# Kernel tuning notes

Hardware: AMD Instinct MI355X
Metric: run time of the kernel (lower is better)

The kernel has to match this reference:

```python
import jax, jax.numpy as jnp
import numpy as np
import math

H = 1024
E = 8
K = 2
CF = 1.5
THR = 0.5


def setup_inputs() -> dict:
    key = jax.random.key(0)
    ks = jax.random.split(key, 8)
    s = 0.02
    return {
        'hidden_states': jax.random.normal(ks[0], (2, 2048, H), jnp.float32),
        # importance predictor: Linear(H, H//2) -> ReLU -> Linear(H//2, 1) -> Sigmoid
        'wi1': jax.random.normal(ks[1], (H, H // 2), jnp.float32) * s,
        'bi1': jnp.zeros((H // 2,), jnp.float32),
        'wi2': jax.random.normal(ks[2], (H // 2, 1), jnp.float32) * s,
        'bi2': jnp.zeros((1,), jnp.float32),
        # router_important: Linear(H,H) -> ReLU -> Linear(H,E)
        'wr1': jax.random.normal(ks[3], (H, H), jnp.float32) * s,
        'br1': jnp.zeros((H,), jnp.float32),
        'wr2': jax.random.normal(ks[4], (H, E), jnp.float32) * s,
        'br2': jnp.zeros((E,), jnp.float32),
        # router_unimportant: Linear(H,H) -> ReLU -> Linear(H,E)
        'wu1': jax.random.normal(ks[5], (H, H), jnp.float32) * s,
        'bu1': jnp.zeros((H,), jnp.float32),
        'wu2': jax.random.normal(ks[6], (H, E), jnp.float32) * s,
        'bu2': jnp.zeros((E,), jnp.float32),
    }


def reference(hidden_states, wi1, bi1, wi2, bi2, wr1, br1, wr2, br2, wu1, bu1, wu2, bu2):
    x = hidden_states
    B, S, _ = x.shape
    N = B * S
    capacity = int(B * S * CF * K / E)  # static per-expert capacity

    # dual-gate routing
    importance = jax.nn.sigmoid(jnp.maximum(x @ wi1 + bi1, 0.0) @ wi2 + bi2)  # [B,S,1]
    imp_mask = (importance > THR).astype(x.dtype)                              # [B,S,1]
    logits_imp = jnp.maximum(x @ wr1 + br1, 0.0) @ wr2 + br2                   # [B,S,E]
    logits_unimp = jnp.maximum(x @ wu1 + bu1, 0.0) @ wu2 + bu2                 # [B,S,E]
    router_logits = imp_mask * logits_imp + (1.0 - imp_mask) * logits_unimp
    router_probs = jax.nn.softmax(router_logits, axis=-1)                      # [B,S,E]

    top_k_probs, top_k_indices = jax.lax.top_k(router_probs, K)
    top_k_probs = top_k_probs / top_k_probs.sum(-1, keepdims=True)

    # capacity-constrained dispatch: k-major assignment order (outer loop over k,
    # tokens in order), position within expert = running count, drop if >= capacity
    ef = top_k_indices.reshape(N, K).T.reshape(-1)   # [K*N] expert id, k-major
    pf = top_k_probs.reshape(N, K).T.reshape(-1)     # [K*N] gate prob
    tf = jnp.tile(jnp.arange(N), K)                  # [K*N] token id
    oh = jax.nn.one_hot(ef, E, dtype=jnp.int32)      # [K*N, E]
    pos = jnp.take_along_axis(jnp.cumsum(oh, axis=0), ef[:, None], 1)[:, 0] - 1
    keep = pos < capacity
    posc = jnp.clip(pos, 0, capacity - 1)

    zeros = jnp.zeros((N, E, capacity), x.dtype)
    dispatch = zeros.at[tf, ef, posc].add(keep.astype(x.dtype))
    combine = zeros.at[tf, ef, posc].add(jnp.where(keep, pf, 0.0))
    dispatch = dispatch.reshape(B, S, E, capacity)
    combine = combine.reshape(B, S, E, capacity)

    # aux losses
    rppe = router_probs.mean((0, 1))
    entropy_loss = jnp.sum(rppe * jnp.log(rppe * E + 1e-9))
    imp_sum = (router_probs * imp_mask).sum((0, 1)) + 1e-9
    ippe = imp_sum / imp_sum.sum()
    imp_entropy = -jnp.sum(ippe * jnp.log(ippe + 1e-9))
    aux_loss = entropy_loss - 0.1 * (imp_entropy / math.log(E))

    return dispatch, combine, router_probs, aux_loss, importance
```

## Files before the change

### kernel.cpp

```cpp
#include <hip/hip_runtime.h>
#include <math.h>

#define HDIM  1024
#define HHALF 512
#define NEXP  8
#define NTOK  4096
#define CAP   1536
#define NTOT  2560
#define TOTAL_DC (2u * NTOK * NEXP * CAP)

typedef _Float16 f16x8 __attribute__((ext_vector_type(8)));
typedef float    f32x4 __attribute__((ext_vector_type(4)));

#define GEMM_BLOCKS 640
#define FILL_BLOCKS 1408
#define S_LO 2048.0f
#define S_W  32.0f

__global__ __launch_bounds__(256) void prep(
    const float* __restrict__ x,
    const float* __restrict__ wi1, const float* __restrict__ wr1,
    const float* __restrict__ wu1,
    const float* __restrict__ bi1, const float* __restrict__ br1,
    const float* __restrict__ bu1,
    _Float16* __restrict__ Ah, _Float16* __restrict__ Al,
    _Float16* __restrict__ Bth, _Float16* __restrict__ Btl,
    float* __restrict__ bias_cat)
{
    __shared__ float tile[64][65];
    const int bid = blockIdx.x, tid = threadIdx.x;

    if (bid < 2048) {
        const int i8 = bid * 256 + tid;
        const float4* x4 = (const float4*)x;
        float4 v0 = x4[i8 * 2];
        float4 v1 = x4[i8 * 2 + 1];
        float f[8] = {v0.x, v0.y, v0.z, v0.w, v1.x, v1.y, v1.z, v1.w};
        f16x8 hi, lo;
#pragma unroll
        for (int j = 0; j < 8; j++) {
            _Float16 h = (_Float16)f[j];
            hi[j] = h;
            lo[j] = (_Float16)((f[j] - (float)h) * S_LO);
        }
        *(f16x8*)&Ah[(size_t)i8 * 8] = hi;
        *(f16x8*)&Al[(size_t)i8 * 8] = lo;
        return;
    }
    if (bid < 2688) {
        int local; const float* src; int C, nof;
        int b = bid - 2048;
        if (b < 128)      { src = wi1; C = 512;  nof = 0;    local = b; }
        else if (b < 384) { src = wr1; C = 1024; nof = 512;  local = b - 128; }
        else              { src = wu1; C = 1024; nof = 1536; local = b - 384; }
        const int nti = local >> 4, kti = local & 15;
#pragma unroll
        for (int p = 0; p < 16; p++) {
            int e = p * 256 + tid;
            int kr = e >> 6, nc = e & 63;
            tile[kr][nc] = src[(size_t)(kti * 64 + kr) * C + nti * 64 + nc];
        }
        __syncthreads();
#pragma unroll
        for (int p = 0; p < 16; p++) {
            int e = p * 256 + tid;
            int nl = e >> 6, kk = e & 63;
            float w32 = tile[kk][nl] * S_W;
            _Float16 h = (_Float16)w32;
            _Float16 l = (_Float16)((w32 - (float)h) * S_LO);
            const size_t o = (size_t)(nof + nti * 64 + nl) * 1024 + kti * 64 + kk;
            Bth[o] = h;
            Btl[o] = l;
        }
        return;
    }
    for (int i = tid; i < NTOT; i += 256) {
        float v = (i < 512) ? bi1[i] : (i < 1536) ? br1[i - 512] : bu1[i - 1536];
        bias_cat[i] = v;
    }
}

__global__ __launch_bounds__(256, 2) void gemm_fill(
    const _Float16* __restrict__ Ah, const _Float16* __restrict__ Al,
    const _Float16* __restrict__ Bth, const _Float16* __restrict__ Btl,
    const float* __restrict__ bias_cat, float* __restrict__ H,
    float* __restrict__ out)
{
    if (blockIdx.x >= GEMM_BLOCKS) {
        float4* o4 = (float4*)out;
        const unsigned total4 = TOTAL_DC / 4;
        unsigned i = (blockIdx.x - GEMM_BLOCKS) * 256u + threadIdx.x;
        const unsigned stride = FILL_BLOCKS * 256u;
        const float4 z = {0.f, 0.f, 0.f, 0.f};
        for (; i < total4; i += stride) o4[i] = z;
        return;
    }

    __shared__ _Float16 lds[4][128][32];

    const int tid = threadIdx.x;
    const int lane = tid & 63, wid = tid >> 6;
    const int bn = blockIdx.x % 20, bm = blockIdx.x / 20;
    const int rowBase = bm * 128, colBase = bn * 128;

    const _Float16* gb =
        (wid == 0) ? Ah  + (size_t)rowBase * 1024 :
        (wid == 1) ? Al  + (size_t)rowBase * 1024 :
        (wid == 2) ? Bth + (size_t)colBase * 1024 :
                     Btl + (size_t)colBase * 1024;
    const int lrow = lane >> 2;
    const int lkg  = lane & 3;

    f32x4 acc_hh[4][4], acc_x[4][4];
    const f32x4 z4 = {0.f, 0.f, 0.f, 0.f};
#pragma unroll
    for (int i = 0; i < 4; i++)
#pragma unroll
        for (int j = 0; j < 4; j++) { acc_hh[i][j] = z4; acc_x[i][j] = z4; }

    const int mw = (wid >> 1) * 64, nw = (wid & 1) * 64;
    const int fr = lane & 15, s = lane >> 4;

    for (int k0 = 0; k0 < 1024; k0 += 32) {
        __syncthreads();
#pragma unroll
        for (int i = 0; i < 8; i++) {
            const int r = i * 16 + lrow;
            __builtin_amdgcn_global_load_lds(
                (const void*)(gb + (size_t)r * 1024 + k0 + lkg * 8),
                (void*)&lds[wid][i * 16][0], 16, 0, 0);
        }
        __syncthreads();

        f16x8 fa_h[4], fa_l[4], fb_h[4], fb_l[4];
#pragma unroll
        for (int mf = 0; mf < 4; mf++) {
            fa_h[mf] = *(const f16x8*)&lds[0][mw + mf * 16 + fr][s * 8];
            fa_l[mf] = *(const f16x8*)&lds[1][mw + mf * 16 + fr][s * 8];
        }
#pragma unroll
        for (int nf = 0; nf < 4; nf++) {
            fb_h[nf] = *(const f16x8*)&lds[2][nw + nf * 16 + fr][s * 8];
            fb_l[nf] = *(const f16x8*)&lds[3][nw + nf * 16 + fr][s * 8];
        }
#pragma unroll
        for (int mf = 0; mf < 4; mf++)
#pragma unroll
            for (int nf = 0; nf < 4; nf++) {
                acc_hh[mf][nf] = __builtin_amdgcn_mfma_f32_16x16x32_f16(
                    fa_h[mf], fb_h[nf], acc_hh[mf][nf], 0, 0, 0);
                acc_x[mf][nf] = __builtin_amdgcn_mfma_f32_16x16x32_f16(
                    fa_h[mf], fb_l[nf], acc_x[mf][nf], 0, 0, 0);
                acc_x[mf][nf] = __builtin_amdgcn_mfma_f32_16x16x32_f16(
                    fa_l[mf], fb_h[nf], acc_x[mf][nf], 0, 0, 0);
            }
    }

#pragma unroll
    for (int mf = 0; mf < 4; mf++) {
        const int row0 = rowBase + mw + mf * 16 + (lane >> 4) * 4;
#pragma unroll
        for (int nf = 0; nf < 4; nf++) {
            const int col = colBase + nw + nf * 16 + (lane & 15);
            const float b = bias_cat[col];
#pragma unroll
            for (int r = 0; r < 4; r++) {
                float v = (acc_hh[mf][nf][r] + acc_x[mf][nf][r] * (1.0f / S_LO))
                          * (1.0f / S_W) + b;
                H[(size_t)(row0 + r) * NTOT + col] = fmaxf(v, 0.f);
            }
        }
    }
}

__global__ __launch_bounds__(256) void second_layer(
    const float* __restrict__ H,
    const float* __restrict__ wi2, const float* __restrict__ bi2,
    const float* __restrict__ wr2, const float* __restrict__ br2,
    const float* __restrict__ wu2, const float* __restrict__ bu2,
    float* __restrict__ oprobs, float* __restrict__ oimp,
    int* __restrict__ tke, float* __restrict__ tkp)
{
    const int t = blockIdx.x;
    const int tid = threadIdx.x;
    const float* hrow = H + (size_t)t * NTOT;

    float pi = 0.f;
    float pr[8], pu[8];
#pragma unroll
    for (int e = 0; e < 8; e++) { pr[e] = 0.f; pu[e] = 0.f; }

    for (int j = tid; j < HHALF; j += 256) pi = fmaf(hrow[j], wi2[j], pi);
    for (int j = tid; j < HDIM; j += 256) {
        float a = hrow[512 + j], b = hrow[1536 + j];
#pragma unroll
        for (int e = 0; e < 8; e++) {
            pr[e] = fmaf(a, wr2[j * 8 + e], pr[e]);
            pu[e] = fmaf(b, wu2[j * 8 + e], pu[e]);
        }
    }

#pragma unroll
    for (int off = 32; off > 0; off >>= 1) {
        pi += __shfl_down(pi, off, 64);
#pragma unroll
        for (int e = 0; e < 8; e++) {
            pr[e] += __shfl_down(pr[e], off, 64);
            pu[e] += __shfl_down(pu[e], off, 64);
        }
    }

    __shared__ float red[4][17];
    const int lane = tid & 63, wv = tid >> 6;
    if (lane == 0) {
        red[wv][0] = pi;
#pragma unroll
        for (int e = 0; e < 8; e++) { red[wv][1 + e] = pr[e]; red[wv][9 + e] = pu[e]; }
    }
    __syncthreads();

    if (tid == 0) {
        float si = red[0][0] + red[1][0] + red[2][0] + red[3][0] + bi2[0];
        float sig = 1.f / (1.f + expf(-si));
        oimp[t] = sig;
        const bool m = sig > 0.5f;
        float lg[8];
#pragma unroll
        for (int e = 0; e < 8; e++) {
            float vr = red[0][1 + e] + red[1][1 + e] + red[2][1 + e] + red[3][1 + e] + br2[e];
            float vu = red[0][9 + e] + red[1][9 + e] + red[2][9 + e] + red[3][9 + e] + bu2[e];
            lg[e] = m ? vr : vu;
        }
        float mx = lg[0];
#pragma unroll
        for (int e = 1; e < 8; e++) mx = fmaxf(mx, lg[e]);
        float p[8], sum = 0.f;
#pragma unroll
        for (int e = 0; e < 8; e++) { p[e] = expf(lg[e] - mx); sum += p[e]; }
        const float inv = 1.f / sum;
#pragma unroll
        for (int e = 0; e < 8; e++) { p[e] *= inv; oprobs[t * 8 + e] = p[e]; }
        int i1 = 0;
#pragma unroll
        for (int e = 1; e < 8; e++) if (p[e] > p[i1]) i1 = e;
        int i2 = (i1 == 0) ? 1 : 0;
#pragma unroll
        for (int e = 0; e < 8; e++) if (e != i1 && p[e] > p[i2]) i2 = e;
        const float ps = p[i1] + p[i2];
        tke[t]        = i1;
        tke[NTOK + t] = i2;
        tkp[t]        = p[i1] / ps;
        tkp[NTOK + t] = p[i2] / ps;
    }
}

__global__ __launch_bounds__(256) void aux_kernel(
    const float* __restrict__ oprobs, const float* __restrict__ oimp,
    float* __restrict__ oaux)
{
    const int tid = threadIdx.x;
    float ap[8], ai[8];
#pragma unroll
    for (int e = 0; e < 8; e++) { ap[e] = 0.f; ai[e] = 0.f; }

    for (int t = tid; t < NTOK; t += 256) {
        const float msk = (oimp[t] > 0.5f) ? 1.f : 0.f;
#pragma unroll
        for (int e = 0; e < 8; e++) {
            float p = oprobs[t * 8 + e];
            ap[e] += p;
            ai[e] = fmaf(msk, p, ai[e]);
        }
    }
#pragma unroll
    for (int off = 32; off > 0; off >>= 1) {
#pragma unroll
        for (int e = 0; e < 8; e++) {
            ap[e] += __shfl_down(ap[e], off, 64);
            ai[e] += __shfl_down(ai[e], off, 64);
        }
    }
    __shared__ float red[4][16];
    const int lane = tid & 63, wv = tid >> 6;
    if (lane == 0) {
#pragma unroll
        for (int e = 0; e < 8; e++) { red[wv][e] = ap[e]; red[wv][8 + e] = ai[e]; }
    }
    __syncthreads();
    if (tid == 0) {
        float ent = 0.f, tot = 0.f, isv[8];
#pragma unroll
        for (int e = 0; e < 8; e++) {
            float sp = red[0][e] + red[1][e] + red[2][e] + red[3][e];
            float sm = red[0][8 + e] + red[1][8 + e] + red[2][8 + e] + red[3][8 + e];
            float r = sp / (float)NTOK;
            ent += r * logf(r * 8.f + 1e-9f);
            isv[e] = sm + 1e-9f;
            tot += isv[e];
        }
        float ie = 0.f;
#pragma unroll
        for (int e = 0; e < 8; e++) {
            float q = isv[e] / tot;
            ie -= q * logf(q + 1e-9f);
        }
        oaux[0] = ent - 0.1f * (ie / logf(8.f));
    }
}

__global__ __launch_bounds__(256) void scan_table(
    const int* __restrict__ tke, const float* __restrict__ tkp,
    float2* __restrict__ table)
{
    __shared__ unsigned char se[2 * NTOK];
    __shared__ float         sp[2 * NTOK];
    __shared__ int cnts[256][8];

    const int tid = threadIdx.x;

    for (int i = tid; i < 2 * NTOK; i += 256) {
        se[i] = (unsigned char)tke[i];
        sp[i] = tkp[i];
    }
    for (int i = tid; i < NTOK * NEXP; i += 256) table[i] = make_float2(-1.f, 0.f);
    __syncthreads();

    const int base = tid * 32;
    int c[8];
#pragma unroll
    for (int e = 0; e < 8; e++) c[e] = 0;
    for (int i = 0; i < 32; i++) {
        int e = se[base + i];
#pragma unroll
        for (int k = 0; k < 8; k++) c[k] += (e == k) ? 1 : 0;
    }
#pragma unroll
    for (int e = 0; e < 8; e++) cnts[tid][e] = c[e];
    __syncthreads();

    if (tid < 8) {
        int run = 0;
        for (int i = 0; i < 256; i++) {
            int v = cnts[i][tid];
            cnts[i][tid] = run;
            run += v;
        }
    }
    __syncthreads();

    int basecnt[8];
#pragma unroll
    for (int e = 0; e < 8; e++) basecnt[e] = cnts[tid][e];

    for (int i = 0; i < 32; i++) {
        const int idx = base + i;
        const int e = se[idx];
        int pos = 0;
#pragma unroll
        for (int k = 0; k < 8; k++)
            if (e == k) { pos = basecnt[k]; basecnt[k]++; }
        if (pos < CAP) {
            const int tok = idx & (NTOK - 1);
            table[tok * NEXP + e] = make_float2((float)pos, sp[idx]);
        }
    }
}

__global__ __launch_bounds__(256) void scatter(
    const float2* __restrict__ table, float* __restrict__ out)
{
    const int i = blockIdx.x * 256 + threadIdx.x;
    const float2 te = table[i];
    if (te.x >= 0.f) {
        const int pos = (int)te.x;
        const size_t o = (size_t)i * CAP + pos;
        out[o] = 1.0f;
        out[(size_t)NTOK * NEXP * CAP + o] = te.y;
    }
}

__global__ __launch_bounds__(256) void gemm_bias_relu(
    const float* __restrict__ A, const float* __restrict__ B,
    const float* __restrict__ bias, float* __restrict__ Hout, int N)
{
    __shared__ float As[16][132];
    __shared__ float Bs[16][132];
    const int tid = threadIdx.x;
    const int tx = tid & 15, ty = tid >> 4;
    const int rowBase = blockIdx.y * 128, colBase = blockIdx.x * 128;
    const int lrow = tid >> 1, lkq = (tid & 1) * 8;
    const int bkk = tid >> 4, bcol = (tid & 15) * 8;
    float acc[8][8];
#pragma unroll
    for (int i = 0; i < 8; i++)
#pragma unroll
        for (int j = 0; j < 8; j++) acc[i][j] = 0.f;
    const float* Aptr = A + (size_t)(rowBase + lrow) * HDIM + lkq;
    const float* Bptr = B + (size_t)bkk * N + colBase + bcol;
    for (int k0 = 0; k0 < HDIM; k0 += 16) {
        float4 a0 = *(const float4*)(Aptr + k0);
        float4 a1 = *(const float4*)(Aptr + k0 + 4);
        float4 b0 = *(const float4*)(Bptr + (size_t)k0 * N);
        float4 b1 = *(const float4*)(Bptr + (size_t)k0 * N + 4);
        __syncthreads();
        As[lkq + 0][lrow] = a0.x; As[lkq + 1][lrow] = a0.y;
        As[lkq + 2][lrow] = a0.z; As[lkq + 3][lrow] = a0.w;
        As[lkq + 4][lrow] = a1.x; As[lkq + 5][lrow] = a1.y;
        As[lkq + 6][lrow] = a1.z; As[lkq + 7][lrow] = a1.w;
        *(float4*)&Bs[bkk][bcol] = b0;
        *(float4*)&Bs[bkk][bcol + 4] = b1;
        __syncthreads();
#pragma unroll
        for (int kk = 0; kk < 16; kk++) {
            float4 x0 = *(const float4*)&As[kk][ty * 8];
            float4 x1 = *(const float4*)&As[kk][ty * 8 + 4];
            float4 y0 = *(const float4*)&Bs[kk][tx * 8];
            float4 y1 = *(const float4*)&Bs[kk][tx * 8 + 4];
            float av[8] = {x0.x, x0.y, x0.z, x0.w, x1.x, x1.y, x1.z, x1.w};
            float bv[8] = {y0.x, y0.y, y0.z, y0.w, y1.x, y1.y, y1.z, y1.w};
#pragma unroll
            for (int i = 0; i < 8; i++)
#pragma unroll
                for (int j = 0; j < 8; j++)
                    acc[i][j] = fmaf(av[i], bv[j], acc[i][j]);
        }
    }
#pragma unroll
    for (int i = 0; i < 8; i++) {
        const int r = rowBase + ty * 8 + i, c = colBase + tx * 8;
#pragma unroll
        for (int j = 0; j < 8; j += 4) {
            float4 v;
            v.x = fmaxf(acc[i][j + 0] + bias[c + j + 0], 0.f);
            v.y = fmaxf(acc[i][j + 1] + bias[c + j + 1], 0.f);
            v.z = fmaxf(acc[i][j + 2] + bias[c + j + 2], 0.f);
            v.w = fmaxf(acc[i][j + 3] + bias[c + j + 3], 0.f);
            *(float4*)&Hout[(size_t)r * N + c + j] = v;
        }
    }
}

__global__ __launch_bounds__(256) void zerofill_fb(float* __restrict__ out)
{
    float4* o4 = (float4*)out;
    const unsigned total4 = TOTAL_DC / 4;
    unsigned i = blockIdx.x * 256u + threadIdx.x;
    const unsigned stride = gridDim.x * 256u;
    const float4 z = {0.f, 0.f, 0.f, 0.f};
    for (; i < total4; i += stride) o4[i] = z;
}

__global__ __launch_bounds__(256) void second_layer_sep(
    const float* __restrict__ h_i, const float* __restrict__ h_r,
    const float* __restrict__ h_u,
    const float* __restrict__ wi2, const float* __restrict__ bi2,
    const float* __restrict__ wr2, const float* __restrict__ br2,
    const float* __restrict__ wu2, const float* __restrict__ bu2,
    float* __restrict__ oprobs, float* __restrict__ oimp,
    int* __restrict__ tke, float* __restrict__ tkp)
{
    const int t = blockIdx.x;
    const int tid = threadIdx.x;
    float pi = 0.f;
    float pr[8], pu[8];
#pragma unroll
    for (int e = 0; e < 8; e++) { pr[e] = 0.f; pu[e] = 0.f; }
    const float* hi = h_i + (size_t)t * HHALF;
    const float* hr = h_r + (size_t)t * HDIM;
    const float* hu = h_u + (size_t)t * HDIM;
    for (int j = tid; j < HHALF; j += 256) pi = fmaf(hi[j], wi2[j], pi);
    for (int j = tid; j < HDIM; j += 256) {
        float a = hr[j], b = hu[j];
#pragma unroll
        for (int e = 0; e < 8; e++) {
            pr[e] = fmaf(a, wr2[j * 8 + e], pr[e]);
            pu[e] = fmaf(b, wu2[j * 8 + e], pu[e]);
        }
    }
#pragma unroll
    for (int off = 32; off > 0; off >>= 1) {
        pi += __shfl_down(pi, off, 64);
#pragma unroll
        for (int e = 0; e < 8; e++) {
            pr[e] += __shfl_down(pr[e], off, 64);
            pu[e] += __shfl_down(pu[e], off, 64);
        }
    }
    __shared__ float red[4][17];
    const int lane = tid & 63, wv = tid >> 6;
    if (lane == 0) {
        red[wv][0] = pi;
#pragma unroll
        for (int e = 0; e < 8; e++) { red[wv][1 + e] = pr[e]; red[wv][9 + e] = pu[e]; }
    }
    __syncthreads();
    if (tid == 0) {
        float si = red[0][0] + red[1][0] + red[2][0] + red[3][0] + bi2[0];
        float sig = 1.f / (1.f + expf(-si));
        oimp[t] = sig;
        const bool m = sig > 0.5f;
        float lg[8];
#pragma unroll
        for (int e = 0; e < 8; e++) {
            float vr = red[0][1 + e] + red[1][1 + e] + red[2][1 + e] + red[3][1 + e] + br2[e];
            float vu = red[0][9 + e] + red[1][9 + e] + red[2][9 + e] + red[3][9 + e] + bu2[e];
            lg[e] = m ? vr : vu;
        }
        float mx = lg[0];
#pragma unroll
        for (int e = 1; e < 8; e++) mx = fmaxf(mx, lg[e]);
        float p[8], s = 0.f;
#pragma unroll
        for (int e = 0; e < 8; e++) { p[e] = expf(lg[e] - mx); s += p[e]; }
        const float inv = 1.f / s;
#pragma unroll
        for (int e = 0; e < 8; e++) { p[e] *= inv; oprobs[t * 8 + e] = p[e]; }
        int i1 = 0;
#pragma unroll
        for (int e = 1; e < 8; e++) if (p[e] > p[i1]) i1 = e;
        int i2 = (i1 == 0) ? 1 : 0;
#pragma unroll
        for (int e = 0; e < 8; e++) if (e != i1 && p[e] > p[i2]) i2 = e;
        const float ps = p[i1] + p[i2];
        tke[t]        = i1;
        tke[NTOK + t] = i2;
        tkp[t]        = p[i1] / ps;
        tkp[NTOK + t] = p[i2] / ps;
    }
}

extern "C" void kernel_launch(void* const* d_in, const int* in_sizes, int n_in,
                              void* d_out, int out_size, void* d_ws, size_t ws_size,
                              hipStream_t stream) {
    const float* x   = (const float*)d_in[0];
    const float* wi1 = (const float*)d_in[1];
    const float* bi1 = (const float*)d_in[2];
    const float* wi2 = (const float*)d_in[3];
    const float* bi2 = (const float*)d_in[4];
    const float* wr1 = (const float*)d_in[5];
    const float* br1 = (const float*)d_in[6];
    const float* wr2 = (const float*)d_in[7];
    const float* br2 = (const float*)d_in[8];
    const float* wu1 = (const float*)d_in[9];
    const float* bu1 = (const float*)d_in[10];
    const float* wu2 = (const float*)d_in[11];
    const float* bu2 = (const float*)d_in[12];

    float* out    = (float*)d_out;
    float* oprobs = out + (size_t)TOTAL_DC;
    float* oaux   = oprobs + NTOK * NEXP;
    float* oimp   = oaux + 1;

    const size_t szH  = (size_t)NTOK * NTOT * 4;
    const size_t szA  = (size_t)NTOK * HDIM * 2;
    const size_t szB  = (size_t)NTOT * HDIM * 2;
    const size_t need = szH + 2 * szA + 2 * szB + NTOT * 4
                      + 2 * NTOK * 4 + 2 * NTOK * 4 + (size_t)NTOK * NEXP * 8 + 4096;
    dim3 blk(256);

    if (ws_size >= need) {
        char* p = (char*)d_ws;
        float*    H    = (float*)p;            p += szH;
        _Float16* Ah   = (_Float16*)p;         p += szA;
        _Float16* Al   = (_Float16*)p;         p += szA;
        _Float16* Bth  = (_Float16*)p;         p += szB;
        _Float16* Btl  = (_Float16*)p;         p += szB;
        float*    bias = (float*)p;            p += NTOT * 4;
        int*      tke  = (int*)p;              p += 2 * NTOK * 4;
        float*    tkp  = (float*)p;            p += 2 * NTOK * 4;
        float2*   table = (float2*)p;

        prep<<<2689, blk, 0, stream>>>(x, wi1, wr1, wu1, bi1, br1, bu1,
                                       Ah, Al, Bth, Btl, bias);
        gemm_fill<<<GEMM_BLOCKS + FILL_BLOCKS, blk, 0, stream>>>(
            Ah, Al, Bth, Btl, bias, H, out);
        second_layer<<<NTOK, blk, 0, stream>>>(H, wi2, bi2, wr2, br2, wu2, bu2,
                                               oprobs, oimp, tke, tkp);
        scan_table<<<1, blk, 0, stream>>>(tke, tkp, table);
        aux_kernel<<<1, blk, 0, stream>>>(oprobs, oimp, oaux);
        scatter<<<128, blk, 0, stream>>>(table, out);
    } else {
        float* h_i = out;
        float* h_r = h_i + (size_t)NTOK * HHALF;
        float* h_u = h_r + (size_t)NTOK * HDIM;
        int*   tke  = (int*)d_ws;
        float* tkp  = (float*)d_ws + 2 * NTOK;
        float2* table = (float2*)((float*)d_ws + 4 * NTOK);

        gemm_bias_relu<<<dim3(HHALF / 128, NTOK / 128), blk, 0, stream>>>(x, wi1, bi1, h_i, HHALF);
        gemm_bias_relu<<<dim3(HDIM / 128, NTOK / 128), blk, 0, stream>>>(x, wr1, br1, h_r, HDIM);
        gemm_bias_relu<<<dim3(HDIM / 128, NTOK / 128), blk, 0, stream>>>(x, wu1, bu1, h_u, HDIM);
        second_layer_sep<<<NTOK, blk, 0, stream>>>(h_i, h_r, h_u, wi2, bi2, wr2, br2,
                                                   wu2, bu2, oprobs, oimp, tke, tkp);
        scan_table<<<1, blk, 0, stream>>>(tke, tkp, table);
        aux_kernel<<<1, blk, 0, stream>>>(oprobs, oimp, oaux);
        zerofill_fb<<<2048, blk, 0, stream>>>(out);
        scatter<<<128, blk, 0, stream>>>(table, out);
    }
}
```

Baseline: 209.7 us.

## Double-buffer GEMM LDS, remap blocks per XCD, nontemporal zero-fill, fuse scan with scatter

The split-fp16 GEMM now double-buffers its LDS tiles, so the next K-slice is fetched while the current one is computed, with one barrier per stage instead of two. Blocks are remapped so each XCD gets a contiguous group of row tiles, which should improve L2 reuse. The zero-fill of the large dispatch/combine output uses nontemporal stores to avoid polluting the cache. The scan and scatter kernels are merged so a single block writes directly into the output, removing the intermediate table and one launch. In exchange, LDS use per block doubles and the scatter is now serialized in one block.

```diff
diff --git a/kernel.cpp b/kernel.cpp
--- a/kernel.cpp
+++ b/kernel.cpp
@@ -87,20 +87,25 @@
     float* __restrict__ out)
 {
     if (blockIdx.x >= GEMM_BLOCKS) {
-        float4* o4 = (float4*)out;
+        f32x4* o4 = (f32x4*)out;
         const unsigned total4 = TOTAL_DC / 4;
         unsigned i = (blockIdx.x - GEMM_BLOCKS) * 256u + threadIdx.x;
         const unsigned stride = FILL_BLOCKS * 256u;
-        const float4 z = {0.f, 0.f, 0.f, 0.f};
-        for (; i < total4; i += stride) o4[i] = z;
+        const f32x4 z = {0.f, 0.f, 0.f, 0.f};
+        for (; i < total4; i += stride)
+            __builtin_nontemporal_store(z, o4 + i);
         return;
     }
 
-    __shared__ _Float16 lds[4][128][32];
+    __shared__ _Float16 lds[2][4][128][32];
 
     const int tid = threadIdx.x;
     const int lane = tid & 63, wid = tid >> 6;
-    const int bn = blockIdx.x % 20, bm = blockIdx.x / 20;
+
+    const int xcd = blockIdx.x & 7;
+    const int idx = blockIdx.x >> 3;
+    const int bm  = xcd * 4 + (idx & 3);
+    const int bn  = idx >> 2;
     const int rowBase = bm * 128, colBase = bn * 128;
 
     const _Float16* gb =
@@ -121,40 +126,56 @@
     const int mw = (wid >> 1) * 64, nw = (wid & 1) * 64;
     const int fr = lane & 15, s = lane >> 4;
 
-    for (int k0 = 0; k0 < 1024; k0 += 32) {
+#define STAGE(buf, k0)                                                        \
+    {                                                                         \
+        _Pragma("unroll")                                                     \
+        for (int i = 0; i < 8; i++) {                                         \
+            const int r = i * 16 + lrow;                                      \
+            __builtin_amdgcn_global_load_lds(                                 \
+                (const void*)(gb + (size_t)r * 1024 + (k0) + lkg * 8),        \
+                (void*)&lds[buf][wid][i * 16][0], 16, 0, 0);                  \
+        }                                                                     \
+    }
+
+#define COMPUTE(buf)                                                          \
+    {                                                                         \
+        f16x8 fa_h[4], fa_l[4], fb_h[4], fb_l[4];                             \
+        _Pragma("unroll")                                                     \
+        for (int mf = 0; mf < 4; mf++) {                                      \
+            fa_h[mf] = *(const f16x8*)&lds[buf][0][mw + mf * 16 + fr][s * 8]; \
+            fa_l[mf] = *(const f16x8*)&lds[buf][1][mw + mf * 16 + fr][s * 8]; \
+        }                                                                     \
+        _Pragma("unroll")                                                     \
+        for (int nf = 0; nf < 4; nf++) {                                      \
+            fb_h[nf] = *(const f16x8*)&lds[buf][2][nw + nf * 16 + fr][s * 8]; \
+            fb_l[nf] = *(const f16x8*)&lds[buf][3][nw + nf * 16 + fr][s * 8]; \
+        }                                                                     \
+        _Pragma("unroll")                                                     \
+        for (int mf = 0; mf < 4; mf++)                                        \
+            _Pragma("unroll")                                                 \
+            for (int nf = 0; nf < 4; nf++) {                                  \
+                acc_hh[mf][nf] = __builtin_amdgcn_mfma_f32_16x16x32_f16(      \
+                    fa_h[mf], fb_h[nf], acc_hh[mf][nf], 0, 0, 0);             \
+                acc_x[mf][nf] = __builtin_amdgcn_mfma_f32_16x16x32_f16(       \
+                    fa_h[mf], fb_l[nf], acc_x[mf][nf], 0, 0, 0);              \
+                acc_x[mf][nf] = __builtin_amdgcn_mfma_f32_16x16x32_f16(       \
+                    fa_l[mf], fb_h[nf], acc_x[mf][nf], 0, 0, 0);              \
+            }                                                                 \
+    }
+
+    STAGE(0, 0);
+    __syncthreads();
+
+    for (int t = 0; t < 32; t += 2) {
+        if (t + 1 < 32) STAGE(1, (t + 1) * 32);
+        COMPUTE(0);
         __syncthreads();
-#pragma unroll
-        for (int i = 0; i < 8; i++) {
-            const int r = i * 16 + lrow;
-            __builtin_amdgcn_global_load_lds(
-                (const void*)(gb + (size_t)r * 1024 + k0 + lkg * 8),
-                (void*)&lds[wid][i * 16][0], 16, 0, 0);
-        }
+        if (t + 2 < 32) STAGE(0, (t + 2) * 32);
+        COMPUTE(1);
         __syncthreads();
-
-        f16x8 fa_h[4], fa_l[4], fb_h[4], fb_l[4];
-#pragma unroll
-        for (int mf = 0; mf < 4; mf++) {
-            fa_h[mf] = *(const f16x8*)&lds[0][mw + mf * 16 + fr][s * 8];
-            fa_l[mf] = *(const f16x8*)&lds[1][mw + mf * 16 + fr][s * 8];
-        }
-#pragma unroll
-        for (int nf = 0; nf < 4; nf++) {
-            fb_h[nf] = *(const f16x8*)&lds[2][nw + nf * 16 + fr][s * 8];
-            fb_l[nf] = *(const f16x8*)&lds[3][nw + nf * 16 + fr][s * 8];
-        }
-#pragma unroll
-        for (int mf = 0; mf < 4; mf++)
-#pragma unroll
-            for (int nf = 0; nf < 4; nf++) {
-                acc_hh[mf][nf] = __builtin_amdgcn_mfma_f32_16x16x32_f16(
-                    fa_h[mf], fb_h[nf], acc_hh[mf][nf], 0, 0, 0);
-                acc_x[mf][nf] = __builtin_amdgcn_mfma_f32_16x16x32_f16(
-                    fa_h[mf], fb_l[nf], acc_x[mf][nf], 0, 0, 0);
-                acc_x[mf][nf] = __builtin_amdgcn_mfma_f32_16x16x32_f16(
-                    fa_l[mf], fb_h[nf], acc_x[mf][nf], 0, 0, 0);
-            }
-    }
+    }
+#undef STAGE
+#undef COMPUTE
 
 #pragma unroll
     for (int mf = 0; mf < 4; mf++) {
@@ -308,9 +329,9 @@
     }
 }
 
-__global__ __launch_bounds__(256) void scan_table(
+__global__ __launch_bounds__(256) void scan_scatter(
     const int* __restrict__ tke, const float* __restrict__ tkp,
-    float2* __restrict__ table)
+    float* __restrict__ out)
 {
     __shared__ unsigned char se[2 * NTOK];
     __shared__ float         sp[2 * NTOK];
@@ -322,7 +343,6 @@
         se[i] = (unsigned char)tke[i];
         sp[i] = tkp[i];
     }
-    for (int i = tid; i < NTOK * NEXP; i += 256) table[i] = make_float2(-1.f, 0.f);
     __syncthreads();
 
     const int base = tid * 32;
@@ -352,6 +372,8 @@
 #pragma unroll
     for (int e = 0; e < 8; e++) basecnt[e] = cnts[tid][e];
 
+    float* comb = out + (size_t)NTOK * NEXP * CAP;
+
     for (int i = 0; i < 32; i++) {
         const int idx = base + i;
         const int e = se[idx];
@@ -361,21 +383,10 @@
             if (e == k) { pos = basecnt[k]; basecnt[k]++; }
         if (pos < CAP) {
             const int tok = idx & (NTOK - 1);
-            table[tok * NEXP + e] = make_float2((float)pos, sp[idx]);
-        }
-    }
-}
-
-__global__ __launch_bounds__(256) void scatter(
-    const float2* __restrict__ table, float* __restrict__ out)
-{
-    const int i = blockIdx.x * 256 + threadIdx.x;
-    const float2 te = table[i];
-    if (te.x >= 0.f) {
-        const int pos = (int)te.x;
-        const size_t o = (size_t)i * CAP + pos;
-        out[o] = 1.0f;
-        out[(size_t)NTOK * NEXP * CAP + o] = te.y;
+            const size_t o = ((size_t)tok * NEXP + e) * CAP + pos;
+            out[o]  = 1.0f;
+            comb[o] = sp[idx];
+        }
     }
 }
 
@@ -442,11 +453,11 @@
 
 __global__ __launch_bounds__(256) void zerofill_fb(float* __restrict__ out)
 {
-    float4* o4 = (float4*)out;
+    f32x4* o4 = (f32x4*)out;
     const unsigned total4 = TOTAL_DC / 4;
     unsigned i = blockIdx.x * 256u + threadIdx.x;
     const unsigned stride = gridDim.x * 256u;
-    const float4 z = {0.f, 0.f, 0.f, 0.f};
+    const f32x4 z = {0.f, 0.f, 0.f, 0.f};
     for (; i < total4; i += stride) o4[i] = z;
 }
 
@@ -555,7 +566,7 @@
     const size_t szA  = (size_t)NTOK * HDIM * 2;
     const size_t szB  = (size_t)NTOT * HDIM * 2;
     const size_t need = szH + 2 * szA + 2 * szB + NTOT * 4
-                      + 2 * NTOK * 4 + 2 * NTOK * 4 + (size_t)NTOK * NEXP * 8 + 4096;
+                      + 2 * NTOK * 4 + 2 * NTOK * 4 + 4096;
     dim3 blk(256);
 
     if (ws_size >= need) {
@@ -567,8 +578,7 @@
         _Float16* Btl  = (_Float16*)p;         p += szB;
         float*    bias = (float*)p;            p += NTOT * 4;
         int*      tke  = (int*)p;              p += 2 * NTOK * 4;
-        float*    tkp  = (float*)p;            p += 2 * NTOK * 4;
-        float2*   table = (float2*)p;
+        float*    tkp  = (float*)p;
 
         prep<<<2689, blk, 0, stream>>>(x, wi1, wr1, wu1, bi1, br1, bu1,
                                        Ah, Al, Bth, Btl, bias);
@@ -576,25 +586,22 @@
             Ah, Al, Bth, Btl, bias, H, out);
         second_layer<<<NTOK, blk, 0, stream>>>(H, wi2, bi2, wr2, br2, wu2, bu2,
                                                oprobs, oimp, tke, tkp);
-        scan_table<<<1, blk, 0, stream>>>(tke, tkp, table);
         aux_kernel<<<1, blk, 0, stream>>>(oprobs, oimp, oaux);
-        scatter<<<128, blk, 0, stream>>>(table, out);
+        scan_scatter<<<1, blk, 0, stream>>>(tke, tkp, out);
     } else {
         float* h_i = out;
         float* h_r = h_i + (size_t)NTOK * HHALF;
         float* h_u = h_r + (size_t)NTOK * HDIM;
         int*   tke  = (int*)d_ws;
         float* tkp  = (float*)d_ws + 2 * NTOK;
-        float2* table = (float2*)((float*)d_ws + 4 * NTOK);
 
         gemm_bias_relu<<<dim3(HHALF / 128, NTOK / 128), blk, 0, stream>>>(x, wi1, bi1, h_i, HHALF);
         gemm_bias_relu<<<dim3(HDIM / 128, NTOK / 128), blk, 0, stream>>>(x, wr1, br1, h_r, HDIM);
         gemm_bias_relu<<<dim3(HDIM / 128, NTOK / 128), blk, 0, stream>>>(x, wu1, bu1, h_u, HDIM);
         second_layer_sep<<<NTOK, blk, 0, stream>>>(h_i, h_r, h_u, wi2, bi2, wr2, br2,
                                                    wu2, bu2, oprobs, oimp, tke, tkp);
-        scan_table<<<1, blk, 0, stream>>>(tke, tkp, table);
         aux_kernel<<<1, blk, 0, stream>>>(oprobs, oimp, oaux);
         zerofill_fb<<<2048, blk, 0, stream>>>(out);
-        scatter<<<128, blk, 0, stream>>>(table, out);
-    }
-}
+        scan_scatter<<<1, blk, 0, stream>>>(tke, tkp, out);
+    }
+}
```

New measurement: 179.0 us. -14.7%, faster.
